# Kernel tuning notes

Hardware: AMD Instinct MI355X
Metric: run time of the kernel (lower is better)

## Reference

```python
import jax, jax.numpy as jnp
import numpy as np

N = 100000
F_IN = 128
HID = 256
NUM_CLASSES = 64
E = 1600000


def setup_inputs() -> dict:
    key = jax.random.key(0)
    ks = jax.random.split(key, 10)
    x = jax.random.normal(ks[0], (N, F_IN), dtype=jnp.float32)
    edge_index = jax.random.randint(ks[1], (2, E), 0, N, dtype=jnp.int32)
    edge_weight = jax.random.uniform(ks[2], (E,), dtype=jnp.float32)
    def glorot(k, shape):
        lim = np.sqrt(6.0 / (shape[0] + shape[1]))
        return jax.random.uniform(k, shape, jnp.float32, -lim, lim)
    W0 = glorot(ks[3], (F_IN, HID)); b0 = jnp.zeros((HID,), jnp.float32)
    W1 = glorot(ks[4], (HID, HID)); b1 = jnp.zeros((HID,), jnp.float32)
    W2 = glorot(ks[5], (HID, NUM_CLASSES)); b2 = jnp.zeros((NUM_CLASSES,), jnp.float32)
    return {"x": x, "edge_index": edge_index, "edge_weight": edge_weight,
            "W0": W0, "b0": b0, "W1": W1, "b1": b1, "W2": W2, "b2": b2}


def _gcn_norm(edge_index, edge_weight, n_nodes):
    # renormalization trick: add self-loops (weight 1), D^-1/2 A D^-1/2
    loop = jnp.arange(n_nodes, dtype=edge_index.dtype)
    src = jnp.concatenate([edge_index[0], loop])
    dst = jnp.concatenate([edge_index[1], loop])
    w = jnp.concatenate([edge_weight, jnp.ones((n_nodes,), edge_weight.dtype)])
    deg = jax.ops.segment_sum(w, dst, num_segments=n_nodes)
    d_inv_sqrt = jnp.where(deg > 0, jax.lax.rsqrt(jnp.maximum(deg, 1e-12)), 0.0)
    norm = d_inv_sqrt[src] * w * d_inv_sqrt[dst]
    return src, dst, norm


def _gcn_layer(x, src, dst, norm, W, b, act):
    h = x @ W                                  # [N, d_out] project first (cheap dense)
    msg = h[src] * norm[:, None]               # [E+N, d_out] gather + scale
    out = jax.ops.segment_sum(msg, dst, num_segments=x.shape[0]) + b
    return act(out) if act is not None else out


def reference(x, edge_index, edge_weight, W0, b0, W1, b1, W2, b2):
    n_nodes = x.shape[0]
    src, dst, norm = _gcn_norm(edge_index, edge_weight, n_nodes)
    # dropout is identity at inference (training=None)
    h = _gcn_layer(x, src, dst, norm, W0, b0, jax.nn.relu)
    h = _gcn_layer(h, src, dst, norm, W1, b1, jax.nn.relu)
    h = _gcn_layer(h, src, dst, norm, W2, b2, None)
    return h
```

## Files before the change

kernel.cpp:

```cpp
#include <hip/hip_runtime.h>

#define N_NODES 100000
#define F_IN 128
#define HID 256
#define NCLS 64
#define N_EDGES 1600000

typedef _Float16 f16;
typedef f16 half8 __attribute__((ext_vector_type(8)));
typedef f16 half4 __attribute__((ext_vector_type(4)));
typedef float f32x4 __attribute__((ext_vector_type(4)));

#define FIXED_SCALE 67108864.0f

__global__ void k_init(unsigned long long* __restrict__ degp, int n) {
    int i = blockIdx.x * 256 + threadIdx.x;
    if (i < n) degp[i] = (unsigned long long)(1u << 26);
}

#define EB   6250
#define XB   12500
#define W0B  128
#define W1B  256
#define W2B  64
__global__ __launch_bounds__(256) void mega1(
        const int* __restrict__ dst, const float* __restrict__ ew,
        unsigned long long* __restrict__ degp, int* __restrict__ seq,
        const float* __restrict__ x, f16* __restrict__ xh,
        const float* __restrict__ W0, f16* __restrict__ Wt0,
        const float* __restrict__ W1, f16* __restrict__ Wt1,
        const float* __restrict__ W2, f16* __restrict__ Wt2) {
    int bid = blockIdx.x;
    int t = threadIdx.x;
    if (bid < EB) {
        int i = bid * 256 + t;
        if (i < N_EDGES) {
            unsigned long long c = (1ULL << 40) |
                (unsigned long long)__float2uint_rn(ew[i] * FIXED_SCALE);
            unsigned long long old = atomicAdd(&degp[dst[i]], c);
            seq[i] = (int)(old >> 40);
        }
    } else if (bid < EB + XB) {
        int i = (bid - EB) * 256 + t;
        if (i < N_NODES * (F_IN / 4)) {
            float4 v = *(const float4*)&x[(size_t)i * 4];
            half4 o;
            o[0] = (f16)v.x; o[1] = (f16)v.y; o[2] = (f16)v.z; o[3] = (f16)v.w;
            *(half4*)&xh[(size_t)i * 4] = o;
        }
    } else if (bid < EB + XB + W0B) {
        int i = (bid - EB - XB) * 256 + t;
        int k = i / HID, d = i % HID;
        Wt0[d * F_IN + k] = (f16)W0[i];
    } else if (bid < EB + XB + W0B + W1B) {
        int i = (bid - EB - XB - W0B) * 256 + t;
        int k = i / HID, d = i % HID;
        Wt1[d * HID + k] = (f16)W1[i];
    } else {
        int i = (bid - EB - XB - W0B - W1B) * 256 + t;
        int k = i / NCLS, d = i % NCLS;
        Wt2[d * HID + k] = (f16)W2[i];
    }
}

__global__ void k_dis(const unsigned long long* __restrict__ degp,
                      float* __restrict__ dis, float* __restrict__ selfnorm,
                      int* __restrict__ cnt, int n) {
    int i = blockIdx.x * 256 + threadIdx.x;
    if (i < n) {
        unsigned long long p = degp[i];
        cnt[i] = (int)(p >> 40);
        float deg = (float)(p & ((1ULL << 40) - 1)) * (1.0f / FIXED_SCALE);
        float d = rsqrtf(deg);
        dis[i] = d;
        selfnorm[i] = d * d;
    }
}

__global__ void k_scan1(const int* __restrict__ cnt, int* __restrict__ incl,
                        int* __restrict__ bsum, int n) {
    __shared__ int s[256];
    int t = threadIdx.x;
    int i = blockIdx.x * 256 + t;
    int v = (i < n) ? cnt[i] : 0;
    s[t] = v;
    __syncthreads();
    #pragma unroll
    for (int off = 1; off < 256; off <<= 1) {
        int x = (t >= off) ? s[t - off] : 0;
        __syncthreads();
        s[t] += x;
        __syncthreads();
    }
    if (i < n) incl[i] = s[t];
    if (t == 255) bsum[blockIdx.x] = s[255];
}

__global__ void k_scan2(const int* __restrict__ bsum, int* __restrict__ boff, int nb) {
    __shared__ int s[512];
    int t = threadIdx.x;
    int v = (t < nb) ? bsum[t] : 0;
    s[t] = v;
    __syncthreads();
    #pragma unroll
    for (int off = 1; off < 512; off <<= 1) {
        int x = (t >= off) ? s[t - off] : 0;
        __syncthreads();
        s[t] += x;
        __syncthreads();
    }
    if (t < nb) boff[t] = s[t] - v;
}

__global__ void k_scan3(int* __restrict__ row, const int* __restrict__ cnt,
                        const int* __restrict__ boff, int n) {
    int i = blockIdx.x * 256 + threadIdx.x;
    if (i < n) row[i] = row[i] - cnt[i] + boff[i >> 8];
}

__global__ void k_place(const int* __restrict__ src, const int* __restrict__ dst,
                        const float* __restrict__ w, const int* __restrict__ seq,
                        const int* __restrict__ row, const float* __restrict__ dis,
                        int2* __restrict__ csr, int e) {
    int i = blockIdx.x * 256 + threadIdx.x;
    if (i < e) {
        int s = src[i], d = dst[i];
        float nw = dis[s] * w[i] * dis[d];
        int pos = row[d] + seq[i];
        csr[pos] = make_int2(s, __float_as_int(nw));
    }
}

template <int K, int DOUT, bool BIAS_RELU>
__global__ __launch_bounds__(256) void gemm_mfma(const f16* __restrict__ in,
                                                 const f16* __restrict__ Wt,
                                                 const float* __restrict__ bias,
                                                 f16* __restrict__ out,
                                                 int nNodes) {
    constexpr int BM = 128, BN = 64, BK = 32;
    constexpr int AP = 40;
    constexpr int CP = 72;
    constexpr int SMEM = (BM * AP + BN * AP) > (BM * CP) ? (BM * AP + BN * AP) : (BM * CP);
    __shared__ f16 smem[SMEM];
    f16* As = smem;
    f16* Bs = smem + BM * AP;

    const int t = threadIdx.x;
    const int w = t >> 6;
    const int lane = t & 63;
    const int quad = lane >> 4;
    const int l16 = lane & 15;
    const int nodeBase = blockIdx.x * BM;
    const int colBase = blockIdx.y * BN;

    f32x4 acc[2][4] = {};

    for (int k0 = 0; k0 < K; k0 += BK) {
        {
            int koff = (t & 3) * 8;
            #pragma unroll
            for (int p = 0; p < 2; ++p) {
                int r = (t >> 2) + p * 64;
                int gn = nodeBase + r;
                if (gn >= nNodes) gn = nNodes - 1;
                half8 v = *(const half8*)&in[(size_t)gn * K + k0 + koff];
                *(half8*)&As[r * AP + koff] = v;
            }
        }
        {
            int koff = (t & 3) * 8;
            int c = t >> 2;
            half8 v = *(const half8*)&Wt[(size_t)(colBase + c) * K + k0 + koff];
            *(half8*)&Bs[c * AP + koff] = v;
        }
        __syncthreads();

        half8 a[2];
        #pragma unroll
        for (int rt = 0; rt < 2; ++rt)
            a[rt] = *(const half8*)&As[(w * 32 + rt * 16 + l16) * AP + quad * 8];
        #pragma unroll
        for (int ct = 0; ct < 4; ++ct) {
            half8 b = *(const half8*)&Bs[(ct * 16 + l16) * AP + quad * 8];
            acc[0][ct] = __builtin_amdgcn_mfma_f32_16x16x32_f16(a[0], b, acc[0][ct], 0, 0, 0);
            acc[1][ct] = __builtin_amdgcn_mfma_f32_16x16x32_f16(a[1], b, acc[1][ct], 0, 0, 0);
        }
        __syncthreads();
    }

    float bv[4];
    #pragma unroll
    for (int ct = 0; ct < 4; ++ct)
        bv[ct] = BIAS_RELU ? bias[colBase + ct * 16 + l16] : 0.0f;

    f16* Cs = smem;
    #pragma unroll
    for (int rt = 0; rt < 2; ++rt)
        #pragma unroll
        for (int ct = 0; ct < 4; ++ct)
            #pragma unroll
            for (int r = 0; r < 4; ++r) {
                int rr = w * 32 + rt * 16 + quad * 4 + r;
                int cc = ct * 16 + l16;
                float v = acc[rt][ct][r];
                if (BIAS_RELU) v = fmaxf(v + bv[ct], 0.0f);
                Cs[rr * CP + cc] = (f16)v;
            }
    __syncthreads();
    #pragma unroll
    for (int p = 0; p < 4; ++p) {
        int r = (t >> 3) + p * 32;
        int gn = nodeBase + r;
        int chunk = (t & 7) * 8;
        if (gn < nNodes)
            *(half8*)&out[(size_t)gn * DOUT + colBase + chunk] =
                *(const half8*)&Cs[r * CP + chunk];
    }
}

template <int DOUT, int TPN, bool HAS_BIAS, bool OUT_F32>
__global__ __launch_bounds__(256) void agg_csr(const f16* __restrict__ h,
                                               const int2* __restrict__ csr,
                                               const int* __restrict__ row,
                                               const int* __restrict__ cnt,
                                               const float* __restrict__ sn,
                                               const float* __restrict__ bias,
                                               void* __restrict__ outv, int nNodes) {
    constexpr int NPB = 256 / TPN;
    int node = blockIdx.x * NPB + threadIdx.x / TPN;
    if (node >= nNodes) return;
    int lane = threadIdx.x % TPN;
    int col = lane * 8;

    float s = sn[node];
    half8 hv = *(const half8*)&h[(size_t)node * DOUT + col];
    float acc[8];
    #pragma unroll
    for (int i = 0; i < 8; ++i)
        acc[i] = s * (float)hv[i] + (HAS_BIAS ? bias[col + i] : 0.0f);

    int e = row[node];
    int end = e + cnt[node];
    for (; e + 1 < end; e += 2) {
        int2 e0 = csr[e], e1 = csr[e + 1];
        float w0 = __int_as_float(e0.y), w1 = __int_as_float(e1.y);
        half8 a0 = *(const half8*)&h[(size_t)e0.x * DOUT + col];
        half8 a1 = *(const half8*)&h[(size_t)e1.x * DOUT + col];
        #pragma unroll
        for (int i = 0; i < 8; ++i) acc[i] += w0 * (float)a0[i] + w1 * (float)a1[i];
    }
    if (e < end) {
        int2 e0 = csr[e];
        float w0 = __int_as_float(e0.y);
        half8 a0 = *(const half8*)&h[(size_t)e0.x * DOUT + col];
        #pragma unroll
        for (int i = 0; i < 8; ++i) acc[i] += w0 * (float)a0[i];
    }

    if (OUT_F32) {
        float* out = (float*)outv;
        float4 r0 = make_float4(acc[0], acc[1], acc[2], acc[3]);
        float4 r1 = make_float4(acc[4], acc[5], acc[6], acc[7]);
        *(float4*)&out[(size_t)node * DOUT + col] = r0;
        *(float4*)&out[(size_t)node * DOUT + col + 4] = r1;
    } else {
        f16* out = (f16*)outv;
        half8 o;
        #pragma unroll
        for (int i = 0; i < 8; ++i) o[i] = (f16)acc[i];
        *(half8*)&out[(size_t)node * DOUT + col] = o;
    }
}

extern "C" void kernel_launch(void* const* d_in, const int* in_sizes, int n_in,
                              void* d_out, int out_size, void* d_ws, size_t ws_size,
                              hipStream_t stream) {
    const float* x  = (const float*)d_in[0];
    const int*   ei = (const int*)d_in[1];
    const float* ew = (const float*)d_in[2];
    const float* W0 = (const float*)d_in[3];
    const float* b0 = (const float*)d_in[4];
    const float* W1 = (const float*)d_in[5];
    const float* b1 = (const float*)d_in[6];
    const float* W2 = (const float*)d_in[7];
    const float* b2 = (const float*)d_in[8];
    const int* src = ei;
    const int* dst = ei + N_EDGES;
    float* outp = (float*)d_out;

    char* ws = (char*)d_ws;
    unsigned long long* degp = (unsigned long long*)ws;  ws += N_NODES * 8;
    int2*  csr      = (int2*)ws;   ws += (size_t)N_EDGES * 8;
    int*   seq      = (int*)ws;    ws += (size_t)N_EDGES * 4;
    float* dis      = (float*)ws;  ws += N_NODES * 4;
    float* selfnorm = (float*)ws;  ws += N_NODES * 4;
    int*   cnt      = (int*)ws;    ws += N_NODES * 4;
    int*   row      = (int*)ws;    ws += N_NODES * 4;
    int*   bsum     = (int*)ws;    ws += 512 * 4;
    int*   boff     = (int*)ws;    ws += 512 * 4;
    f16*   xh       = (f16*)ws;    ws += (size_t)N_NODES * F_IN * 2;
    f16*   Wt0      = (f16*)ws;    ws += F_IN * HID * 2;
    f16*   Wt1      = (f16*)ws;    ws += HID * HID * 2;
    f16*   Wt2      = (f16*)ws;    ws += HID * NCLS * 2;
    f16*   bufA     = (f16*)ws;    ws += (size_t)N_NODES * HID * 2;
    f16*   bufB     = (f16*)ws;    ws += (size_t)N_NODES * HID * 2;

    const int nb = (N_NODES + 255) / 256;
    const int eb = (N_EDGES + 255) / 256;

    k_init<<<nb, 256, 0, stream>>>(degp, N_NODES);
    mega1<<<EB + XB + W0B + W1B + W2B, 256, 0, stream>>>(
        dst, ew, degp, seq, x, xh, W0, Wt0, W1, Wt1, W2, Wt2);
    k_dis<<<nb, 256, 0, stream>>>(degp, dis, selfnorm, cnt, N_NODES);
    k_scan1<<<nb, 256, 0, stream>>>(cnt, row, bsum, N_NODES);
    k_scan2<<<1, 512, 0, stream>>>(bsum, boff, nb);
    k_scan3<<<nb, 256, 0, stream>>>(row, cnt, boff, N_NODES);
    k_place<<<eb, 256, 0, stream>>>(src, dst, ew, seq, row, dis, csr, N_EDGES);

    const int gX = (N_NODES + 127) / 128;

    agg_csr<F_IN, 16, false, false><<<(N_NODES + 15) / 16, 256, 0, stream>>>(
        xh, csr, row, cnt, selfnorm, nullptr, bufA, N_NODES);
    gemm_mfma<F_IN, HID, true><<<dim3(gX, HID / 64), 256, 0, stream>>>(bufA, Wt0, b0, bufB, N_NODES);

    agg_csr<HID, 32, false, false><<<(N_NODES + 7) / 8, 256, 0, stream>>>(
        bufB, csr, row, cnt, selfnorm, nullptr, bufA, N_NODES);
    gemm_mfma<HID, HID, true><<<dim3(gX, HID / 64), 256, 0, stream>>>(bufA, Wt1, b1, bufB, N_NODES);

    gemm_mfma<HID, NCLS, false><<<dim3(gX, NCLS / 64), 256, 0, stream>>>(bufB, Wt2, nullptr, bufA, N_NODES);
    agg_csr<NCLS, 8, true, true><<<(N_NODES + 31) / 32, 256, 0, stream>>>(
        bufA, csr, row, cnt, selfnorm, b2, outp, N_NODES);
}
```

Measured before the change: 554.0 us.

## Fuse degree/scan kernels, remap GEMM blocks per XCD, unroll CSR gather with nontemporal access

```diff
diff --git a/kernel.cpp b/kernel.cpp
--- a/kernel.cpp
+++ b/kernel.cpp
@@ -10,6 +10,7 @@
 typedef f16 half8 __attribute__((ext_vector_type(8)));
 typedef f16 half4 __attribute__((ext_vector_type(4)));
 typedef float f32x4 __attribute__((ext_vector_type(4)));
+typedef unsigned long long u64;
 
 #define FIXED_SCALE 67108864.0f
 
@@ -63,26 +64,23 @@
     }
 }
 
-__global__ void k_dis(const unsigned long long* __restrict__ degp,
-                      float* __restrict__ dis, float* __restrict__ selfnorm,
-                      int* __restrict__ cnt, int n) {
-    int i = blockIdx.x * 256 + threadIdx.x;
+__global__ void k_scan1(const unsigned long long* __restrict__ degp,
+                        int* __restrict__ cnt, float* __restrict__ dis,
+                        float* __restrict__ selfnorm,
+                        int* __restrict__ incl, int* __restrict__ bsum, int n) {
+    __shared__ int s[256];
+    int t = threadIdx.x;
+    int i = blockIdx.x * 256 + t;
+    int v = 0;
     if (i < n) {
         unsigned long long p = degp[i];
-        cnt[i] = (int)(p >> 40);
+        v = (int)(p >> 40);
+        cnt[i] = v;
         float deg = (float)(p & ((1ULL << 40) - 1)) * (1.0f / FIXED_SCALE);
         float d = rsqrtf(deg);
         dis[i] = d;
         selfnorm[i] = d * d;
     }
-}
-
-__global__ void k_scan1(const int* __restrict__ cnt, int* __restrict__ incl,
-                        int* __restrict__ bsum, int n) {
-    __shared__ int s[256];
-    int t = threadIdx.x;
-    int i = blockIdx.x * 256 + t;
-    int v = (i < n) ? cnt[i] : 0;
     s[t] = v;
     __syncthreads();
     #pragma unroll
@@ -138,6 +136,7 @@
                                                  f16* __restrict__ out,
                                                  int nNodes) {
     constexpr int BM = 128, BN = 64, BK = 32;
+    constexpr int NB = DOUT / BN;
     constexpr int AP = 40;
     constexpr int CP = 72;
     constexpr int SMEM = (BM * AP + BN * AP) > (BM * CP) ? (BM * AP + BN * AP) : (BM * CP);
@@ -145,13 +144,19 @@
     f16* As = smem;
     f16* Bs = smem + BM * AP;
 
+    const int nwg = gridDim.x;
+    const int b = blockIdx.x;
+    const int q = nwg >> 3, r = nwg & 7, xcd = b & 7;
+    const int wk = (xcd < r ? xcd * (q + 1) : r * (q + 1) + (xcd - r) * q) + (b >> 3);
+    const int bx = wk / NB, by = wk % NB;
+
     const int t = threadIdx.x;
     const int w = t >> 6;
     const int lane = t & 63;
     const int quad = lane >> 4;
     const int l16 = lane & 15;
-    const int nodeBase = blockIdx.x * BM;
-    const int colBase = blockIdx.y * BN;
+    const int nodeBase = bx * BM;
+    const int colBase = by * BN;
 
     f32x4 acc[2][4] = {};
 
@@ -160,11 +165,11 @@
             int koff = (t & 3) * 8;
             #pragma unroll
             for (int p = 0; p < 2; ++p) {
-                int r = (t >> 2) + p * 64;
-                int gn = nodeBase + r;
+                int r2 = (t >> 2) + p * 64;
+                int gn = nodeBase + r2;
                 if (gn >= nNodes) gn = nNodes - 1;
                 half8 v = *(const half8*)&in[(size_t)gn * K + k0 + koff];
-                *(half8*)&As[r * AP + koff] = v;
+                *(half8*)&As[r2 * AP + koff] = v;
             }
         }
         {
@@ -181,9 +186,9 @@
             a[rt] = *(const half8*)&As[(w * 32 + rt * 16 + l16) * AP + quad * 8];
         #pragma unroll
         for (int ct = 0; ct < 4; ++ct) {
-            half8 b = *(const half8*)&Bs[(ct * 16 + l16) * AP + quad * 8];
-            acc[0][ct] = __builtin_amdgcn_mfma_f32_16x16x32_f16(a[0], b, acc[0][ct], 0, 0, 0);
-            acc[1][ct] = __builtin_amdgcn_mfma_f32_16x16x32_f16(a[1], b, acc[1][ct], 0, 0, 0);
+            half8 bf = *(const half8*)&Bs[(ct * 16 + l16) * AP + quad * 8];
+            acc[0][ct] = __builtin_amdgcn_mfma_f32_16x16x32_f16(a[0], bf, acc[0][ct], 0, 0, 0);
+            acc[1][ct] = __builtin_amdgcn_mfma_f32_16x16x32_f16(a[1], bf, acc[1][ct], 0, 0, 0);
         }
         __syncthreads();
     }
@@ -199,22 +204,22 @@
         #pragma unroll
         for (int ct = 0; ct < 4; ++ct)
             #pragma unroll
-            for (int r = 0; r < 4; ++r) {
-                int rr = w * 32 + rt * 16 + quad * 4 + r;
+            for (int rr2 = 0; rr2 < 4; ++rr2) {
+                int rr = w * 32 + rt * 16 + quad * 4 + rr2;
                 int cc = ct * 16 + l16;
-                float v = acc[rt][ct][r];
+                float v = acc[rt][ct][rr2];
                 if (BIAS_RELU) v = fmaxf(v + bv[ct], 0.0f);
                 Cs[rr * CP + cc] = (f16)v;
             }
     __syncthreads();
     #pragma unroll
     for (int p = 0; p < 4; ++p) {
-        int r = (t >> 3) + p * 32;
-        int gn = nodeBase + r;
+        int rr = (t >> 3) + p * 32;
+        int gn = nodeBase + rr;
         int chunk = (t & 7) * 8;
         if (gn < nNodes)
             *(half8*)&out[(size_t)gn * DOUT + colBase + chunk] =
-                *(const half8*)&Cs[r * CP + chunk];
+                *(const half8*)&Cs[rr * CP + chunk];
     }
 }
 
@@ -241,34 +246,59 @@
 
     int e = row[node];
     int end = e + cnt[node];
+    const u64* csr64 = (const u64*)csr;
+
+    for (; e + 3 < end; e += 4) {
+        u64 p0 = __builtin_nontemporal_load(csr64 + e);
+        u64 p1 = __builtin_nontemporal_load(csr64 + e + 1);
+        u64 p2 = __builtin_nontemporal_load(csr64 + e + 2);
+        u64 p3 = __builtin_nontemporal_load(csr64 + e + 3);
+        const half8 a0 = *(const half8*)&h[(size_t)(unsigned)(p0 & 0xffffffffu) * DOUT + col];
+        const half8 a1 = *(const half8*)&h[(size_t)(unsigned)(p1 & 0xffffffffu) * DOUT + col];
+        const half8 a2 = *(const half8*)&h[(size_t)(unsigned)(p2 & 0xffffffffu) * DOUT + col];
+        const half8 a3 = *(const half8*)&h[(size_t)(unsigned)(p3 & 0xffffffffu) * DOUT + col];
+        float w0 = __int_as_float((int)(p0 >> 32));
+        float w1 = __int_as_float((int)(p1 >> 32));
+        float w2 = __int_as_float((int)(p2 >> 32));
+        float w3 = __int_as_float((int)(p3 >> 32));
+        #pragma unroll
+        for (int i = 0; i < 8; ++i)
+            acc[i] += w0 * (float)a0[i] + w1 * (float)a1[i]
+                    + w2 * (float)a2[i] + w3 * (float)a3[i];
+    }
     for (; e + 1 < end; e += 2) {
-        int2 e0 = csr[e], e1 = csr[e + 1];
-        float w0 = __int_as_float(e0.y), w1 = __int_as_float(e1.y);
-        half8 a0 = *(const half8*)&h[(size_t)e0.x * DOUT + col];
-        half8 a1 = *(const half8*)&h[(size_t)e1.x * DOUT + col];
-        #pragma unroll
-        for (int i = 0; i < 8; ++i) acc[i] += w0 * (float)a0[i] + w1 * (float)a1[i];
+        u64 p0 = __builtin_nontemporal_load(csr64 + e);
+        u64 p1 = __builtin_nontemporal_load(csr64 + e + 1);
+        const half8 a0 = *(const half8*)&h[(size_t)(unsigned)(p0 & 0xffffffffu) * DOUT + col];
+        const half8 a1 = *(const half8*)&h[(size_t)(unsigned)(p1 & 0xffffffffu) * DOUT + col];
+        float w0 = __int_as_float((int)(p0 >> 32));
+        float w1 = __int_as_float((int)(p1 >> 32));
+        #pragma unroll
+        for (int i = 0; i < 8; ++i)
+            acc[i] += w0 * (float)a0[i] + w1 * (float)a1[i];
     }
     if (e < end) {
-        int2 e0 = csr[e];
-        float w0 = __int_as_float(e0.y);
-        half8 a0 = *(const half8*)&h[(size_t)e0.x * DOUT + col];
+        u64 p0 = __builtin_nontemporal_load(csr64 + e);
+        const half8 a0 = *(const half8*)&h[(size_t)(unsigned)(p0 & 0xffffffffu) * DOUT + col];
+        float w0 = __int_as_float((int)(p0 >> 32));
         #pragma unroll
         for (int i = 0; i < 8; ++i) acc[i] += w0 * (float)a0[i];
     }
 
     if (OUT_F32) {
         float* out = (float*)outv;
-        float4 r0 = make_float4(acc[0], acc[1], acc[2], acc[3]);
-        float4 r1 = make_float4(acc[4], acc[5], acc[6], acc[7]);
-        *(float4*)&out[(size_t)node * DOUT + col] = r0;
-        *(float4*)&out[(size_t)node * DOUT + col + 4] = r1;
+        f32x4 r0, r1;
+        r0[0] = acc[0]; r0[1] = acc[1]; r0[2] = acc[2]; r0[3] = acc[3];
+        r1[0] = acc[4]; r1[1] = acc[5]; r1[2] = acc[6]; r1[3] = acc[7];
+        __builtin_nontemporal_store(r0, (f32x4*)&out[(size_t)node * DOUT + col]);
+        __builtin_nontemporal_store(r1, (f32x4*)&out[(size_t)node * DOUT + col + 4]);
     } else {
         f16* out = (f16*)outv;
         half8 o;
         #pragma unroll
         for (int i = 0; i < 8; ++i) o[i] = (f16)acc[i];
-        *(half8*)&out[(size_t)node * DOUT + col] = o;
+        __builtin_nontemporal_store(*(const f32x4*)&o,
+                                    (f32x4*)&out[(size_t)node * DOUT + col]);
     }
 }
 
@@ -311,8 +341,7 @@
     k_init<<<nb, 256, 0, stream>>>(degp, N_NODES);
     mega1<<<EB + XB + W0B + W1B + W2B, 256, 0, stream>>>(
         dst, ew, degp, seq, x, xh, W0, Wt0, W1, Wt1, W2, Wt2);
-    k_dis<<<nb, 256, 0, stream>>>(degp, dis, selfnorm, cnt, N_NODES);
-    k_scan1<<<nb, 256, 0, stream>>>(cnt, row, bsum, N_NODES);
+    k_scan1<<<nb, 256, 0, stream>>>(degp, cnt, dis, selfnorm, row, bsum, N_NODES);
     k_scan2<<<1, 512, 0, stream>>>(bsum, boff, nb);
     k_scan3<<<nb, 256, 0, stream>>>(row, cnt, boff, N_NODES);
     k_place<<<eb, 256, 0, stream>>>(src, dst, ew, seq, row, dis, csr, N_EDGES);
@@ -321,13 +350,13 @@
 
     agg_csr<F_IN, 16, false, false><<<(N_NODES + 15) / 16, 256, 0, stream>>>(
         xh, csr, row, cnt, selfnorm, nullptr, bufA, N_NODES);
-    gemm_mfma<F_IN, HID, true><<<dim3(gX, HID / 64), 256, 0, stream>>>(bufA, Wt0, b0, bufB, N_NODES);
+    gemm_mfma<F_IN, HID, true><<<gX * (HID / 64), 256, 0, stream>>>(bufA, Wt0, b0, bufB, N_NODES);
 
     agg_csr<HID, 32, false, false><<<(N_NODES + 7) / 8, 256, 0, stream>>>(
         bufB, csr, row, cnt, selfnorm, nullptr, bufA, N_NODES);
-    gemm_mfma<HID, HID, true><<<dim3(gX, HID / 64), 256, 0, stream>>>(bufA, Wt1, b1, bufB, N_NODES);
-
-    gemm_mfma<HID, NCLS, false><<<dim3(gX, NCLS / 64), 256, 0, stream>>>(bufB, Wt2, nullptr, bufA, N_NODES);
+    gemm_mfma<HID, HID, true><<<gX * (HID / 64), 256, 0, stream>>>(bufA, Wt1, b1, bufB, N_NODES);
+
+    gemm_mfma<HID, NCLS, false><<<gX * (NCLS / 64), 256, 0, stream>>>(bufB, Wt2, nullptr, bufA, N_NODES);
     agg_csr<NCLS, 8, true, true><<<(N_NODES + 31) / 32, 256, 0, stream>>>(
         bufA, csr, row, cnt, selfnorm, b2, outp, N_NODES);
 }
```

Measured after the change: 555.6 us. Within noise of the previous version (+0.3%).
